# Optimization experiments

Hardware: AMD Instinct MI355X
Metric: run time of the kernel (lower is better)

Reference implementation:

```python
import jax, jax.numpy as jnp
import numpy as np

HEADS, DIM_HEAD, C, B, HS, WS = 8, 64, 512, 2, 48, 48


def setup_inputs() -> dict:
    key = jax.random.key(0)
    ks = jax.random.split(key, 9)
    s = 0.02
    return {
        "hidden_states": jax.random.normal(ks[0], (B, C, HS, WS), jnp.float32),
        "Wq": jax.random.normal(ks[1], (HEADS, DIM_HEAD, C), jnp.float32) * s,
        "bq": jax.random.normal(ks[2], (HEADS, DIM_HEAD), jnp.float32) * s,
        "Wk": jax.random.normal(ks[3], (HEADS, DIM_HEAD, C), jnp.float32) * s,
        "bk": jax.random.normal(ks[4], (HEADS, DIM_HEAD), jnp.float32) * s,
        "Wv": jax.random.normal(ks[5], (HEADS, DIM_HEAD, C), jnp.float32) * s,
        "bv": jax.random.normal(ks[6], (HEADS, DIM_HEAD), jnp.float32) * s,
        "Wo": jax.random.normal(ks[7], (C, HEADS * DIM_HEAD), jnp.float32) * s,
        "bo": jax.random.normal(ks[8], (C,), jnp.float32) * s,
    }


def reference(hidden_states, Wq, bq, Wk, bk, Wv, bv, Wo, bo):
    # hidden_states: [B, C, H, W]; per-head 1x1 convs == per-head linear over C.
    b, c, h, w = hidden_states.shape
    hw = h * w
    x = hidden_states.reshape(b, c, hw)  # [B, C, HW]
    # Batched per-head projections (fuses the per-head Conv2d loop).
    q = jnp.einsum('bcs,ndc->bnsd', x, Wq) + bq[None, :, None, :]  # [B, n, HW, d]
    k = jnp.einsum('bcs,ndc->bnsd', x, Wk) + bk[None, :, None, :]
    v = jnp.einsum('bcs,ndc->bnsd', x, Wv) + bv[None, :, None, :]
    scale = 1.0 / jnp.sqrt(jnp.asarray(DIM_HEAD, hidden_states.dtype))
    scores = jnp.einsum('bnqd,bnkd->bnqk', q, k) * scale  # [B, n, HW, HW]
    probs = jax.nn.softmax(scores, axis=-1)
    attn = jnp.einsum('bnqk,bnkd->bnqd', probs, v)  # [B, n, HW, d]
    # concat heads along last dim (matches torch.cat(..., dim=-1))
    attn = attn.transpose(0, 2, 1, 3).reshape(b, hw, HEADS * DIM_HEAD)
    out = attn @ Wo.T + bo  # [B, HW, C] (to_out[0]; to_out[1] dropout = identity)
    out = out.reshape(b, h, w, c).transpose(0, 3, 1, 2)  # [B, C, H, W]
    return out
```

## Files before the change

kernel.cpp:

```cpp
#include <hip/hip_runtime.h>
#include <hip/hip_bf16.h>

#define HEADS 8
#define DHEAD 64
#define CDIM  512
#define SEQ   2304
#define ND    512

typedef unsigned short u16;
typedef unsigned int   u32;
typedef __attribute__((ext_vector_type(8))) short short8;
typedef __attribute__((ext_vector_type(4))) float f32x4;

#define QSCALE 0.18033688011112043f

__device__ __forceinline__ u16 f2bf(float f) {
    union { float f; u32 u; } x; x.f = f;
    u32 r = x.u + 0x7FFFu + ((x.u >> 16) & 1u);
    return (u16)(r >> 16);
}
__device__ __forceinline__ float bf2f(u16 v) {
    union { u32 u; float f; } x; x.u = ((u32)v) << 16; return x.f;
}
__device__ __forceinline__ u32 pkbf(float a, float b) {
    union { float f; u32 u; } x, y; x.f = a; y.f = b;
    return __builtin_amdgcn_perm(y.u + 0x8000u, x.u + 0x8000u, 0x07060302u);
}
__device__ __forceinline__ f32x4 mfma16(short8 a, short8 b, f32x4 c) {
    return __builtin_amdgcn_mfma_f32_16x16x32_bf16(a, b, c, 0, 0, 0);
}
__device__ __forceinline__ void cp16(const void* g, void* l) {
    __builtin_amdgcn_global_load_lds(
        (const __attribute__((address_space(1))) u32*)(uintptr_t)g,
        (__attribute__((address_space(3))) u32*)(u32)(uintptr_t)l,
        16, 0, 0);
}
__device__ __forceinline__ int kperm_inv(int r) {
    return (r & ~0x1C) | ((r & 0x0C) << 1) | ((r & 0x10) >> 2);
}

__global__ void prep_kernel(const float* __restrict__ H,
                            const float* __restrict__ Wq, const float* __restrict__ Wk,
                            const float* __restrict__ Wv, const float* __restrict__ Wo,
                            u16* __restrict__ Wqkv, u16* __restrict__ Wob,
                            u16* __restrict__ X) {
    __shared__ float tile[32][33];
    const int t = threadIdx.x;
    const int bx = blockIdx.x;
    if (bx < 4096) {
        int idx = bx * 256 + t;
        const int N1 = CDIM * ND;
        if (idx < N1)             Wqkv[idx] = f2bf(Wq[idx]);
        else if (idx < 2 * N1)    Wqkv[idx] = f2bf(Wk[idx - N1]);
        else if (idx < 3 * N1)    Wqkv[idx] = f2bf(Wv[idx - 2 * N1]);
        else                      Wob[idx - 3 * N1] = f2bf(Wo[idx - 3 * N1]);
    } else {
        int bb = bx - 4096;
        int st = bb % 72, ct = (bb / 72) % 16, b = bb / (72 * 16);
        int tx = t & 31, ty = t >> 5;
#pragma unroll
        for (int k = 0; k < 4; ++k) {
            int c = ct * 32 + ty + k * 8;
            tile[ty + k * 8][tx] = H[((size_t)b * CDIM + c) * SEQ + st * 32 + tx];
        }
        __syncthreads();
#pragma unroll
        for (int k = 0; k < 4; ++k) {
            int s = st * 32 + ty + k * 8;
            X[((size_t)b * SEQ + s) * CDIM + ct * 32 + tx] = f2bf(tile[tx][ty + k * 8]);
        }
    }
}

__global__ __launch_bounds__(256) void gemm_qkv_kernel(
        const u16* __restrict__ W, const u16* __restrict__ X,
        const float* __restrict__ bq, const float* __restrict__ bk, const float* __restrict__ bv,
        u16* __restrict__ Q, u16* __restrict__ K, u16* __restrict__ V) {
    __shared__ __align__(16) u16 As[128 * 64];
    __shared__ __align__(16) u16 Bs[128 * 64];
    const int n0 = blockIdx.x * 128;
    const int m0 = blockIdx.y * 128;
    const int b  = blockIdx.z;
    const int t = threadIdx.x;
    const int lane = t & 63, w = t >> 6;
    const int l16 = lane & 15, quad = lane >> 4;
    const int x7 = l16 & 7;
    const int wm = (w >> 1) * 64, wn = (w & 1) * 64;
    const int srow = t >> 3, scol = (t & 7) * 8;
    const int scol_sw = ((t & 7) ^ (srow & 7)) * 8;
    const u16* Xb = X + (size_t)b * SEQ * CDIM;

    f32x4 acc[4][4] = {};

    for (int kb = 0; kb < 512; kb += 64) {
        __syncthreads();
#pragma unroll
        for (int it = 0; it < 4; ++it) {
            int r2 = it * 32 + srow;
            cp16(&W [(size_t)(m0 + r2) * 512 + kb + scol_sw], &As[r2 * 64 + scol]);
            cp16(&Xb[(size_t)(n0 + r2) * 512 + kb + scol_sw], &Bs[r2 * 64 + scol]);
        }
        __syncthreads();
#pragma unroll
        for (int kk = 0; kk < 2; ++kk) {
            const int co = ((kk * 4 + quad) ^ x7) * 8;
            short8 af[4], bfr[4];
#pragma unroll
            for (int i = 0; i < 4; ++i)
                af[i] = *(const short8*)&As[(wm + i * 16 + l16) * 64 + co];
#pragma unroll
            for (int j = 0; j < 4; ++j)
                bfr[j] = *(const short8*)&Bs[(wn + j * 16 + l16) * 64 + co];
#pragma unroll
            for (int i = 0; i < 4; ++i)
#pragma unroll
                for (int j = 0; j < 4; ++j)
                    acc[i][j] = mfma16(af[i], bfr[j], acc[i][j]);
        }
    }

    if (m0 < 1024) {
        const bool isQ = (m0 < 512);
        const float* bias = isQ ? bq : bk;
        const float sc = isQ ? QSCALE : 1.0f;
        const int mq = isQ ? m0 : m0 - 512;
        u16* dst = isQ ? Q : K;
#pragma unroll
        for (int j = 0; j < 4; ++j) {
            int s = n0 + wn + j * 16 + l16;
#pragma unroll
            for (int i = 0; i < 4; ++i) {
                int mm = mq + wm + i * 16 + quad * 4;
                uint2 val;
                val.x = pkbf((acc[i][j][0] + bias[mm + 0]) * sc, (acc[i][j][1] + bias[mm + 1]) * sc);
                val.y = pkbf((acc[i][j][2] + bias[mm + 2]) * sc, (acc[i][j][3] + bias[mm + 3]) * sc);
                *(uint2*)&dst[(((size_t)(b * 8 + (mm >> 6))) * SEQ + s) * 64 + (mm & 63)] = val;
            }
        }
    } else {
#pragma unroll
        for (int j = 0; j < 4; ++j) {
            int s = n0 + wn + j * 16 + l16;
#pragma unroll
            for (int i = 0; i < 4; ++i) {
                int mbase = m0 - 1024 + wm + i * 16 + quad * 4;
#pragma unroll
                for (int r = 0; r < 4; ++r) {
                    int mm = mbase + r;
                    V[((size_t)(b * 512 + mm)) * SEQ + s] = f2bf(acc[i][j][r] + bv[mm]);
                }
            }
        }
    }
}

__global__ __launch_bounds__(256) void attn_partial(
        const u16* __restrict__ Q,
        const u16* __restrict__ K,
        const u16* __restrict__ Vt,
        u16* __restrict__ Opart,
        float* __restrict__ Lpart) {
    __shared__ __align__(16) u16 sm[2 * 64 * 64];
    u16* Ks = sm;
    u16* Vs = sm + 64 * 64;
    const int pair = blockIdx.x & 15, qt = blockIdx.x >> 4;
    const int c = blockIdx.y;
    const int b = pair >> 3, h = pair & 7;
    const int t = threadIdx.x, lane = t & 63, w = t >> 6;
    const int l16 = lane & 15, quad = lane >> 4;
    const int x7 = l16 & 7;
    const int srow = t >> 3;
    const int scol = (t & 7) * 8;
    const int scol_sw = ((t & 7) ^ (srow & 7)) * 8;
    const int kinv0 = kperm_inv(srow), kinv1 = kperm_inv(32 + srow);
    const int cA = (quad ^ x7) * 8;
    const int cB = (quad ^ x7 ^ 4) * 8;

    const u16* Qg = Q + ((size_t)pair * SEQ + qt * 128) * 64;
    const int rA = w * 16 + l16, rB = 64 + rA;
    short8 qfa0 = *(const short8*)&Qg[(size_t)rA * 64 + quad * 8];
    short8 qfa1 = *(const short8*)&Qg[(size_t)rA * 64 + 32 + quad * 8];
    short8 qfb0 = *(const short8*)&Qg[(size_t)rB * 64 + quad * 8];
    short8 qfb1 = *(const short8*)&Qg[(size_t)rB * 64 + 32 + quad * 8];

    const u16* Kg = K  + ((size_t)pair * SEQ + c * 576) * 64;
    const u16* Vg = Vt + ((size_t)(b * 512 + h * 64)) * SEQ + c * 576;

    f32x4 laccA = {0.f, 0.f, 0.f, 0.f}, laccB = {0.f, 0.f, 0.f, 0.f};
    f32x4 oA[4] = {}, oB[4] = {};

    for (int kt = 0; kt < 9; ++kt) {
        __syncthreads();
        cp16(&Kg[(size_t)(kt * 64 + kinv0) * 64 + scol_sw], &Ks[srow * 64 + scol]);
        cp16(&Kg[(size_t)(kt * 64 + kinv1) * 64 + scol_sw], &Ks[(32 + srow) * 64 + scol]);
        cp16(&Vg[(size_t)srow * SEQ + kt * 64 + scol_sw],        &Vs[srow * 64 + scol]);
        cp16(&Vg[(size_t)(32 + srow) * SEQ + kt * 64 + scol_sw], &Vs[(32 + srow) * 64 + scol]);
        __syncthreads();
        f32x4 saccA[4] = {}, saccB[4] = {};
#pragma unroll
        for (int j = 0; j < 4; ++j) {
            short8 kf0 = *(const short8*)&Ks[(j * 16 + l16) * 64 + cA];
            short8 kf1 = *(const short8*)&Ks[(j * 16 + l16) * 64 + cB];
            saccA[j] = mfma16(kf0, qfa0, saccA[j]);
            saccA[j] = mfma16(kf1, qfa1, saccA[j]);
            saccB[j] = mfma16(kf0, qfb0, saccB[j]);
            saccB[j] = mfma16(kf1, qfb1, saccB[j]);
        }
        float pA[4][4], pB[4][4];
#pragma unroll
        for (int j = 0; j < 4; ++j)
#pragma unroll
            for (int r = 0; r < 4; ++r) {
                pA[j][r] = __builtin_amdgcn_exp2f(saccA[j][r]);
                laccA[j] += pA[j][r];
                pB[j][r] = __builtin_amdgcn_exp2f(saccB[j][r]);
                laccB[j] += pB[j][r];
            }
#pragma unroll
        for (int g = 0; g < 2; ++g) {
            short8 pfA, pfB;
            u32* pwA = (u32*)&pfA;
            u32* pwB = (u32*)&pfB;
            pwA[0] = pkbf(pA[2 * g][0], pA[2 * g][1]);
            pwA[1] = pkbf(pA[2 * g][2], pA[2 * g][3]);
            pwA[2] = pkbf(pA[2 * g + 1][0], pA[2 * g + 1][1]);
            pwA[3] = pkbf(pA[2 * g + 1][2], pA[2 * g + 1][3]);
            pwB[0] = pkbf(pB[2 * g][0], pB[2 * g][1]);
            pwB[1] = pkbf(pB[2 * g][2], pB[2 * g][3]);
            pwB[2] = pkbf(pB[2 * g + 1][0], pB[2 * g + 1][1]);
            pwB[3] = pkbf(pB[2 * g + 1][2], pB[2 * g + 1][3]);
            const int cg = g ? cB : cA;
#pragma unroll
            for (int i = 0; i < 4; ++i) {
                short8 vf = *(const short8*)&Vs[(i * 16 + l16) * 64 + cg];
                oA[i] = mfma16(vf, pfA, oA[i]);
                oB[i] = mfma16(vf, pfB, oB[i]);
            }
        }
    }
    float lA = laccA[0] + laccA[1] + laccA[2] + laccA[3];
    lA += __shfl_xor(lA, 16); lA += __shfl_xor(lA, 32);
    float lB = laccB[0] + laccB[1] + laccB[2] + laccB[3];
    lB += __shfl_xor(lB, 16); lB += __shfl_xor(lB, 32);
    float invA = 1.0f / lA, invB = 1.0f / lB;
    const size_t orow = ((size_t)(c * 16 + pair)) * SEQ + qt * 128;

    __syncthreads();
#pragma unroll
    for (int i = 0; i < 4; ++i) {
        uint2 pk;
        pk.x = pkbf(oA[i][0] * invA, oA[i][1] * invA);
        pk.y = pkbf(oA[i][2] * invA, oA[i][3] * invA);
        *(uint2*)&sm[(w * 16 + l16) * 72 + i * 16 + quad * 4] = pk;
    }
    if (quad == 0) Lpart[orow + w * 16 + l16] = lA;
    __syncthreads();
#pragma unroll
    for (int it = 0; it < 2; ++it) {
        int v = it * 256 + t;
        int row = v >> 3, col = (v & 7) * 8;
        *(uint4*)&Opart[(orow + row) * 64 + col] = *(const uint4*)&sm[row * 72 + col];
    }
    __syncthreads();
#pragma unroll
    for (int i = 0; i < 4; ++i) {
        uint2 pk;
        pk.x = pkbf(oB[i][0] * invB, oB[i][1] * invB);
        pk.y = pkbf(oB[i][2] * invB, oB[i][3] * invB);
        *(uint2*)&sm[(w * 16 + l16) * 72 + i * 16 + quad * 4] = pk;
    }
    if (quad == 0) Lpart[orow + 64 + w * 16 + l16] = lB;
    __syncthreads();
#pragma unroll
    for (int it = 0; it < 2; ++it) {
        int v = it * 256 + t;
        int row = v >> 3, col = (v & 7) * 8;
        *(uint4*)&Opart[(orow + 64 + row) * 64 + col] = *(const uint4*)&sm[row * 72 + col];
    }
}

__global__ __launch_bounds__(256) void attn_combine(
        const u16* __restrict__ Opart, const float* __restrict__ Lpart,
        u16* __restrict__ At) {
    const int bid = blockIdx.x;
    const int pair = bid / 144, sb = bid % 144;
    const int tid = threadIdx.x;
    const int rl = tid >> 4, dg = tid & 15;
    const int s = sb * 16 + rl;
    const int b = pair >> 3, h = pair & 7;
    float wc[4], L = 0.f;
#pragma unroll
    for (int c = 0; c < 4; ++c) {
        wc[c] = Lpart[(size_t)(c * 16 + pair) * SEQ + s];
        L += wc[c];
    }
    float invL = 1.0f / L;
    float acc[4] = {0.f, 0.f, 0.f, 0.f};
#pragma unroll
    for (int c = 0; c < 4; ++c) {
        ushort4 v = *(const ushort4*)&Opart[((size_t)(c * 16 + pair) * SEQ + s) * 64 + dg * 4];
        acc[0] += wc[c] * bf2f(v.x);
        acc[1] += wc[c] * bf2f(v.y);
        acc[2] += wc[c] * bf2f(v.z);
        acc[3] += wc[c] * bf2f(v.w);
    }
    uint2 outv;
    outv.x = pkbf(acc[0] * invL, acc[1] * invL);
    outv.y = pkbf(acc[2] * invL, acc[3] * invL);
    *(uint2*)&At[((size_t)b * SEQ + s) * ND + h * 64 + dg * 4] = outv;
}

__global__ __launch_bounds__(256) void gemm_out_kernel(
        const u16* __restrict__ Wob, const u16* __restrict__ At,
        const float* __restrict__ bo, float* __restrict__ out) {
    __shared__ __align__(16) u16 As[64 * 64];
    __shared__ __align__(16) u16 Bs[128 * 64];
    const int n0 = blockIdx.x * 128;
    const int m0 = blockIdx.y * 64;
    const int b  = blockIdx.z;
    const int t = threadIdx.x;
    const int lane = t & 63, w = t >> 6;
    const int l16 = lane & 15, quad = lane >> 4;
    const int x7 = l16 & 7;
    const int srow = t >> 3, scol = (t & 7) * 8;
    const int scol_sw = ((t & 7) ^ (srow & 7)) * 8;
    const u16* Ab = At + (size_t)b * SEQ * ND;

    f32x4 acc[4][2] = {};

    for (int kb = 0; kb < 512; kb += 64) {
        __syncthreads();
#pragma unroll
        for (int it = 0; it < 2; ++it) {
            int r2 = it * 32 + srow;
            cp16(&Wob[(size_t)(m0 + r2) * 512 + kb + scol_sw], &As[r2 * 64 + scol]);
        }
#pragma unroll
        for (int it = 0; it < 4; ++it) {
            int r2 = it * 32 + srow;
            cp16(&Ab[(size_t)(n0 + r2) * 512 + kb + scol_sw], &Bs[r2 * 64 + scol]);
        }
        __syncthreads();
#pragma unroll
        for (int kk = 0; kk < 2; ++kk) {
            const int co = ((kk * 4 + quad) ^ x7) * 8;
            short8 af[4], bfr[2];
#pragma unroll
            for (int i = 0; i < 4; ++i)
                af[i] = *(const short8*)&As[(i * 16 + l16) * 64 + co];
#pragma unroll
            for (int j = 0; j < 2; ++j)
                bfr[j] = *(const short8*)&Bs[(w * 32 + j * 16 + l16) * 64 + co];
#pragma unroll
            for (int i = 0; i < 4; ++i)
#pragma unroll
                for (int j = 0; j < 2; ++j)
                    acc[i][j] = mfma16(af[i], bfr[j], acc[i][j]);
        }
    }
#pragma unroll
    for (int i = 0; i < 4; ++i) {
        int cbase = m0 + i * 16 + quad * 4;
#pragma unroll
        for (int j = 0; j < 2; ++j) {
            int s = n0 + w * 32 + j * 16 + l16;
#pragma unroll
            for (int r = 0; r < 4; ++r) {
                int cc = cbase + r;
                out[((size_t)(b * 512 + cc)) * SEQ + s] = acc[i][j][r] + bo[cc];
            }
        }
    }
}

extern "C" void kernel_launch(void* const* d_in, const int* in_sizes, int n_in,
                              void* d_out, int out_size, void* d_ws, size_t ws_size,
                              hipStream_t stream) {
    const float* H  = (const float*)d_in[0];
    const float* Wq = (const float*)d_in[1];
    const float* bq = (const float*)d_in[2];
    const float* Wk = (const float*)d_in[3];
    const float* bk = (const float*)d_in[4];
    const float* Wv = (const float*)d_in[5];
    const float* bv = (const float*)d_in[6];
    const float* Wo = (const float*)d_in[7];
    const float* bo = (const float*)d_in[8];
    float* out = (float*)d_out;

    u16* ws    = (u16*)d_ws;
    u16* Wqkv  = ws;
    u16* Wob   = Wqkv  + 1536 * 512;
    u16* Xbf   = Wob   + 512 * 512;
    u16* Qb    = Xbf   + 2 * SEQ * CDIM;
    u16* Kb    = Qb    + 2 * SEQ * ND;
    u16* Vb    = Kb    + 2 * SEQ * ND;
    u16* At    = Vb    + 2 * SEQ * ND;
    u16* Opart = At    + 2 * SEQ * ND;
    float* Lpart = (float*)(Opart + 4 * 16 * SEQ * 64);

    prep_kernel<<<6400, 256, 0, stream>>>(H, Wq, Wk, Wv, Wo, Wqkv, Wob, Xbf);
    gemm_qkv_kernel<<<dim3(18, 12, 2), 256, 0, stream>>>(Wqkv, Xbf, bq, bk, bv, Qb, Kb, Vb);
    attn_partial<<<dim3(288, 4), 256, 0, stream>>>(Qb, Kb, Vb, Opart, Lpart);
    attn_combine<<<2304, 256, 0, stream>>>(Opart, Lpart, At);
    gemm_out_kernel<<<dim3(18, 8, 2), 256, 0, stream>>>(Wob, At, bo, out);
}
```

Before: 140.2 us.

## Double-buffer LDS in GEMMs and attention, shrink GEMM tiles for more blocks

Adds ping-pong shared-memory buffers to the QKV GEMM, the attention partial kernel and the output GEMM, so the next tile's async copy is issued before computing on the current one. This removes one barrier per iteration. It also halves the tile sizes of both GEMMs (QKV M tile 128→64, output N tile 128→64), doubling grid size to improve CU fill on the 256-CU part. The attention epilogue now writes both halves in one staged pass. The cost is less data reuse per block and more LDS per block, which may lower occupancy.

```diff
diff --git a/kernel.cpp b/kernel.cpp
--- a/kernel.cpp
+++ b/kernel.cpp
@@ -76,45 +76,66 @@
         const u16* __restrict__ W, const u16* __restrict__ X,
         const float* __restrict__ bq, const float* __restrict__ bk, const float* __restrict__ bv,
         u16* __restrict__ Q, u16* __restrict__ K, u16* __restrict__ V) {
-    __shared__ __align__(16) u16 As[128 * 64];
-    __shared__ __align__(16) u16 Bs[128 * 64];
+    __shared__ __align__(16) u16 sm[2 * (64 * 64 + 128 * 64)];
     const int n0 = blockIdx.x * 128;
-    const int m0 = blockIdx.y * 128;
+    const int m0 = blockIdx.y * 64;
     const int b  = blockIdx.z;
     const int t = threadIdx.x;
     const int lane = t & 63, w = t >> 6;
     const int l16 = lane & 15, quad = lane >> 4;
     const int x7 = l16 & 7;
-    const int wm = (w >> 1) * 64, wn = (w & 1) * 64;
     const int srow = t >> 3, scol = (t & 7) * 8;
     const int scol_sw = ((t & 7) ^ (srow & 7)) * 8;
     const u16* Xb = X + (size_t)b * SEQ * CDIM;
 
-    f32x4 acc[4][4] = {};
-
-    for (int kb = 0; kb < 512; kb += 64) {
-        __syncthreads();
+    f32x4 acc[4][2] = {};
+
+    {
+        u16* As = sm; u16* Bs = sm + 64 * 64;
+#pragma unroll
+        for (int it = 0; it < 2; ++it) {
+            int r2 = it * 32 + srow;
+            cp16(&W[(size_t)(m0 + r2) * 512 + scol_sw], &As[r2 * 64 + scol]);
+        }
 #pragma unroll
         for (int it = 0; it < 4; ++it) {
             int r2 = it * 32 + srow;
-            cp16(&W [(size_t)(m0 + r2) * 512 + kb + scol_sw], &As[r2 * 64 + scol]);
-            cp16(&Xb[(size_t)(n0 + r2) * 512 + kb + scol_sw], &Bs[r2 * 64 + scol]);
-        }
+            cp16(&Xb[(size_t)(n0 + r2) * 512 + scol_sw], &Bs[r2 * 64 + scol]);
+        }
+    }
+    for (int kb = 0; kb < 512; kb += 64) {
+        const int pb = (kb >> 6) & 1;
+        u16* As = sm + pb * 12288;
+        u16* Bs = As + 64 * 64;
         __syncthreads();
+        if (kb + 64 < 512) {
+            u16* An = sm + (pb ^ 1) * 12288;
+            u16* Bn = An + 64 * 64;
+#pragma unroll
+            for (int it = 0; it < 2; ++it) {
+                int r2 = it * 32 + srow;
+                cp16(&W[(size_t)(m0 + r2) * 512 + kb + 64 + scol_sw], &An[r2 * 64 + scol]);
+            }
+#pragma unroll
+            for (int it = 0; it < 4; ++it) {
+                int r2 = it * 32 + srow;
+                cp16(&Xb[(size_t)(n0 + r2) * 512 + kb + 64 + scol_sw], &Bn[r2 * 64 + scol]);
+            }
+        }
 #pragma unroll
         for (int kk = 0; kk < 2; ++kk) {
             const int co = ((kk * 4 + quad) ^ x7) * 8;
-            short8 af[4], bfr[4];
+            short8 af[4], bfr[2];
 #pragma unroll
             for (int i = 0; i < 4; ++i)
-                af[i] = *(const short8*)&As[(wm + i * 16 + l16) * 64 + co];
-#pragma unroll
-            for (int j = 0; j < 4; ++j)
-                bfr[j] = *(const short8*)&Bs[(wn + j * 16 + l16) * 64 + co];
+                af[i] = *(const short8*)&As[(i * 16 + l16) * 64 + co];
+#pragma unroll
+            for (int j = 0; j < 2; ++j)
+                bfr[j] = *(const short8*)&Bs[(w * 32 + j * 16 + l16) * 64 + co];
 #pragma unroll
             for (int i = 0; i < 4; ++i)
 #pragma unroll
-                for (int j = 0; j < 4; ++j)
+                for (int j = 0; j < 2; ++j)
                     acc[i][j] = mfma16(af[i], bfr[j], acc[i][j]);
         }
     }
@@ -126,11 +147,11 @@
         const int mq = isQ ? m0 : m0 - 512;
         u16* dst = isQ ? Q : K;
 #pragma unroll
-        for (int j = 0; j < 4; ++j) {
-            int s = n0 + wn + j * 16 + l16;
+        for (int j = 0; j < 2; ++j) {
+            int s = n0 + w * 32 + j * 16 + l16;
 #pragma unroll
             for (int i = 0; i < 4; ++i) {
-                int mm = mq + wm + i * 16 + quad * 4;
+                int mm = mq + i * 16 + quad * 4;
                 uint2 val;
                 val.x = pkbf((acc[i][j][0] + bias[mm + 0]) * sc, (acc[i][j][1] + bias[mm + 1]) * sc);
                 val.y = pkbf((acc[i][j][2] + bias[mm + 2]) * sc, (acc[i][j][3] + bias[mm + 3]) * sc);
@@ -139,11 +160,11 @@
         }
     } else {
 #pragma unroll
-        for (int j = 0; j < 4; ++j) {
-            int s = n0 + wn + j * 16 + l16;
+        for (int j = 0; j < 2; ++j) {
+            int s = n0 + w * 32 + j * 16 + l16;
 #pragma unroll
             for (int i = 0; i < 4; ++i) {
-                int mbase = m0 - 1024 + wm + i * 16 + quad * 4;
+                int mbase = m0 - 1024 + i * 16 + quad * 4;
 #pragma unroll
                 for (int r = 0; r < 4; ++r) {
                     int mm = mbase + r;
@@ -160,9 +181,7 @@
         const u16* __restrict__ Vt,
         u16* __restrict__ Opart,
         float* __restrict__ Lpart) {
-    __shared__ __align__(16) u16 sm[2 * 64 * 64];
-    u16* Ks = sm;
-    u16* Vs = sm + 64 * 64;
+    __shared__ __align__(16) u16 sm[2 * 8192];
     const int pair = blockIdx.x & 15, qt = blockIdx.x >> 4;
     const int c = blockIdx.y;
     const int b = pair >> 3, h = pair & 7;
@@ -189,13 +208,26 @@
     f32x4 laccA = {0.f, 0.f, 0.f, 0.f}, laccB = {0.f, 0.f, 0.f, 0.f};
     f32x4 oA[4] = {}, oB[4] = {};
 
+    {
+        u16* Ks = sm; u16* Vs = sm + 4096;
+        cp16(&Kg[(size_t)kinv0 * 64 + scol_sw], &Ks[srow * 64 + scol]);
+        cp16(&Kg[(size_t)kinv1 * 64 + scol_sw], &Ks[(32 + srow) * 64 + scol]);
+        cp16(&Vg[(size_t)srow * SEQ + scol_sw],        &Vs[srow * 64 + scol]);
+        cp16(&Vg[(size_t)(32 + srow) * SEQ + scol_sw], &Vs[(32 + srow) * 64 + scol]);
+    }
     for (int kt = 0; kt < 9; ++kt) {
+        const int pb = kt & 1;
+        const u16* Ks = sm + pb * 8192;
+        const u16* Vs = Ks + 4096;
         __syncthreads();
-        cp16(&Kg[(size_t)(kt * 64 + kinv0) * 64 + scol_sw], &Ks[srow * 64 + scol]);
-        cp16(&Kg[(size_t)(kt * 64 + kinv1) * 64 + scol_sw], &Ks[(32 + srow) * 64 + scol]);
-        cp16(&Vg[(size_t)srow * SEQ + kt * 64 + scol_sw],        &Vs[srow * 64 + scol]);
-        cp16(&Vg[(size_t)(32 + srow) * SEQ + kt * 64 + scol_sw], &Vs[(32 + srow) * 64 + scol]);
-        __syncthreads();
+        if (kt < 8) {
+            u16* Kn = sm + (pb ^ 1) * 8192;
+            u16* Vn = Kn + 4096;
+            cp16(&Kg[(size_t)((kt + 1) * 64 + kinv0) * 64 + scol_sw], &Kn[srow * 64 + scol]);
+            cp16(&Kg[(size_t)((kt + 1) * 64 + kinv1) * 64 + scol_sw], &Kn[(32 + srow) * 64 + scol]);
+            cp16(&Vg[(size_t)srow * SEQ + (kt + 1) * 64 + scol_sw],        &Vn[srow * 64 + scol]);
+            cp16(&Vg[(size_t)(32 + srow) * SEQ + (kt + 1) * 64 + scol_sw], &Vn[(32 + srow) * 64 + scol]);
+        }
         f32x4 saccA[4] = {}, saccB[4] = {};
 #pragma unroll
         for (int j = 0; j < 4; ++j) {
@@ -248,34 +280,24 @@
     __syncthreads();
 #pragma unroll
     for (int i = 0; i < 4; ++i) {
-        uint2 pk;
-        pk.x = pkbf(oA[i][0] * invA, oA[i][1] * invA);
-        pk.y = pkbf(oA[i][2] * invA, oA[i][3] * invA);
-        *(uint2*)&sm[(w * 16 + l16) * 72 + i * 16 + quad * 4] = pk;
-    }
-    if (quad == 0) Lpart[orow + w * 16 + l16] = lA;
+        uint2 pka, pkb;
+        pka.x = pkbf(oA[i][0] * invA, oA[i][1] * invA);
+        pka.y = pkbf(oA[i][2] * invA, oA[i][3] * invA);
+        pkb.x = pkbf(oB[i][0] * invB, oB[i][1] * invB);
+        pkb.y = pkbf(oB[i][2] * invB, oB[i][3] * invB);
+        *(uint2*)&sm[(w * 16 + l16) * 72 + i * 16 + quad * 4] = pka;
+        *(uint2*)&sm[(64 + w * 16 + l16) * 72 + i * 16 + quad * 4] = pkb;
+    }
+    if (quad == 0) {
+        Lpart[orow + w * 16 + l16] = lA;
+        Lpart[orow + 64 + w * 16 + l16] = lB;
+    }
     __syncthreads();
 #pragma unroll
-    for (int it = 0; it < 2; ++it) {
+    for (int it = 0; it < 4; ++it) {
         int v = it * 256 + t;
         int row = v >> 3, col = (v & 7) * 8;
         *(uint4*)&Opart[(orow + row) * 64 + col] = *(const uint4*)&sm[row * 72 + col];
-    }
-    __syncthreads();
-#pragma unroll
-    for (int i = 0; i < 4; ++i) {
-        uint2 pk;
-        pk.x = pkbf(oB[i][0] * invB, oB[i][1] * invB);
-        pk.y = pkbf(oB[i][2] * invB, oB[i][3] * invB);
-        *(uint2*)&sm[(w * 16 + l16) * 72 + i * 16 + quad * 4] = pk;
-    }
-    if (quad == 0) Lpart[orow + 64 + w * 16 + l16] = lB;
-    __syncthreads();
-#pragma unroll
-    for (int it = 0; it < 2; ++it) {
-        int v = it * 256 + t;
-        int row = v >> 3, col = (v & 7) * 8;
-        *(uint4*)&Opart[(orow + 64 + row) * 64 + col] = *(const uint4*)&sm[row * 72 + col];
     }
 }
 
@@ -313,9 +335,8 @@
 __global__ __launch_bounds__(256) void gemm_out_kernel(
         const u16* __restrict__ Wob, const u16* __restrict__ At,
         const float* __restrict__ bo, float* __restrict__ out) {
-    __shared__ __align__(16) u16 As[64 * 64];
-    __shared__ __align__(16) u16 Bs[128 * 64];
-    const int n0 = blockIdx.x * 128;
+    __shared__ __align__(16) u16 sm[2 * 8192];
+    const int n0 = blockIdx.x * 64;
     const int m0 = blockIdx.y * 64;
     const int b  = blockIdx.z;
     const int t = threadIdx.x;
@@ -326,49 +347,53 @@
     const int scol_sw = ((t & 7) ^ (srow & 7)) * 8;
     const u16* Ab = At + (size_t)b * SEQ * ND;
 
-    f32x4 acc[4][2] = {};
-
-    for (int kb = 0; kb < 512; kb += 64) {
-        __syncthreads();
+    f32x4 acc[4] = {};
+
+    {
+        u16* As = sm; u16* Bs = sm + 4096;
 #pragma unroll
         for (int it = 0; it < 2; ++it) {
             int r2 = it * 32 + srow;
-            cp16(&Wob[(size_t)(m0 + r2) * 512 + kb + scol_sw], &As[r2 * 64 + scol]);
-        }
-#pragma unroll
-        for (int it = 0; it < 4; ++it) {
-            int r2 = it * 32 + srow;
-            cp16(&Ab[(size_t)(n0 + r2) * 512 + kb + scol_sw], &Bs[r2 * 64 + scol]);
-        }
+            cp16(&Wob[(size_t)(m0 + r2) * 512 + scol_sw], &As[r2 * 64 + scol]);
+            cp16(&Ab [(size_t)(n0 + r2) * 512 + scol_sw], &Bs[r2 * 64 + scol]);
+        }
+    }
+    for (int kb = 0; kb < 512; kb += 64) {
+        const int pb = (kb >> 6) & 1;
+        const u16* As = sm + pb * 8192;
+        const u16* Bs = As + 4096;
         __syncthreads();
+        if (kb + 64 < 512) {
+            u16* An = sm + (pb ^ 1) * 8192;
+            u16* Bn = An + 4096;
+#pragma unroll
+            for (int it = 0; it < 2; ++it) {
+                int r2 = it * 32 + srow;
+                cp16(&Wob[(size_t)(m0 + r2) * 512 + kb + 64 + scol_sw], &An[r2 * 64 + scol]);
+                cp16(&Ab [(size_t)(n0 + r2) * 512 + kb + 64 + scol_sw], &Bn[r2 * 64 + scol]);
+            }
+        }
 #pragma unroll
         for (int kk = 0; kk < 2; ++kk) {
             const int co = ((kk * 4 + quad) ^ x7) * 8;
-            short8 af[4], bfr[2];
+            short8 af[4];
 #pragma unroll
             for (int i = 0; i < 4; ++i)
                 af[i] = *(const short8*)&As[(i * 16 + l16) * 64 + co];
-#pragma unroll
-            for (int j = 0; j < 2; ++j)
-                bfr[j] = *(const short8*)&Bs[(w * 32 + j * 16 + l16) * 64 + co];
+            short8 bfr = *(const short8*)&Bs[(w * 16 + l16) * 64 + co];
 #pragma unroll
             for (int i = 0; i < 4; ++i)
-#pragma unroll
-                for (int j = 0; j < 2; ++j)
-                    acc[i][j] = mfma16(af[i], bfr[j], acc[i][j]);
+                acc[i] = mfma16(af[i], bfr, acc[i]);
         }
     }
 #pragma unroll
     for (int i = 0; i < 4; ++i) {
         int cbase = m0 + i * 16 + quad * 4;
-#pragma unroll
-        for (int j = 0; j < 2; ++j) {
-            int s = n0 + w * 32 + j * 16 + l16;
-#pragma unroll
-            for (int r = 0; r < 4; ++r) {
-                int cc = cbase + r;
-                out[((size_t)(b * 512 + cc)) * SEQ + s] = acc[i][j][r] + bo[cc];
-            }
+        int s = n0 + w * 16 + l16;
+#pragma unroll
+        for (int r = 0; r < 4; ++r) {
+            int cc = cbase + r;
+            out[((size_t)(b * 512 + cc)) * SEQ + s] = acc[i][r] + bo[cc];
         }
     }
 }
@@ -399,8 +424,8 @@
     float* Lpart = (float*)(Opart + 4 * 16 * SEQ * 64);
 
     prep_kernel<<<6400, 256, 0, stream>>>(H, Wq, Wk, Wv, Wo, Wqkv, Wob, Xbf);
-    gemm_qkv_kernel<<<dim3(18, 12, 2), 256, 0, stream>>>(Wqkv, Xbf, bq, bk, bv, Qb, Kb, Vb);
+    gemm_qkv_kernel<<<dim3(18, 24, 2), 256, 0, stream>>>(Wqkv, Xbf, bq, bk, bv, Qb, Kb, Vb);
     attn_partial<<<dim3(288, 4), 256, 0, stream>>>(Qb, Kb, Vb, Opart, Lpart);
     attn_combine<<<2304, 256, 0, stream>>>(Opart, Lpart, At);
-    gemm_out_kernel<<<dim3(18, 8, 2), 256, 0, stream>>>(Wob, At, bo, out);
-}
+    gemm_out_kernel<<<dim3(36, 8, 2), 256, 0, stream>>>(Wob, At, bo, out);
+}
```

Result: faster. 135.8 us (-3.1%).
